# Kernel tuning notes

Hardware: AMD Instinct MI355X
Metric: run time of the kernel (lower is better)

Reference implementation:

```python
import jax, jax.numpy as jnp
import numpy as np

B, H, D = 2048, 4, 4096   # batch, num_heads_h, dim
M = 8                      # groups_m

def setup_inputs() -> dict:
    key = jax.random.key(0)
    ks = jax.random.split(key, 5)
    return {
        "x": jax.random.normal(ks[0], (B, H, D), dtype=jnp.float32),
        "local_W": jax.random.normal(ks[1], (M, H), dtype=jnp.float32) * 0.5,
        "local_b": jax.random.normal(ks[2], (M,), dtype=jnp.float32) * 0.02,
        "proj_W": jax.random.normal(ks[3], (D, D), dtype=jnp.float32) * 0.02,
        "proj_b": jax.random.normal(ks[4], (D,), dtype=jnp.float32) * 0.02,
    }

def reference(x, local_W, local_b, proj_W, proj_b):
    b, h, d = x.shape
    m = local_W.shape[0]
    dm = d // m
    # s: (m, B, dm, h)  -- matches reshape(B,h,m,-1).permute(2,0,3,1)
    s = jnp.transpose(x.reshape(b, h, m, dm), (2, 0, 3, 1))
    # grouped tiny linear (Linear(h,1) per group), all fused in one einsum
    s_out = jnp.einsum('mbch,mh->mbc', s, local_W) + local_b[:, None, None]
    # faithful to torch: cat along dim 0 then reshape(B, D) (group-major flatten)
    s_out = s_out.reshape(b, d)
    out = jax.nn.sigmoid(s_out @ proj_W.T + proj_b)
    return out
```

## Files before the change

### kernel.cpp

```cpp
#include <hip/hip_runtime.h>


#define MD 2048
#define ND 4096
#define KD 4096

typedef __attribute__((ext_vector_type(8))) __bf16 bf16x8;
typedef __attribute__((ext_vector_type(4))) float f32x4;

static __device__ __forceinline__ unsigned short f2bf(float f) {
  union { float f; unsigned int u; } v; v.f = f;
  unsigned int u = v.u;
  u += 0x7FFFu + ((u >> 16) & 1u);
  return (unsigned short)(u >> 16);
}

__global__ __launch_bounds__(256) void prep_kernel(
    const float* __restrict__ x, const float* __restrict__ lW,
    const float* __restrict__ lb, const float* __restrict__ pW,
    unsigned short* __restrict__ sB, unsigned short* __restrict__ wB) {
  int bid = blockIdx.x;
  int tid = threadIdx.x;
  if (bid < 4096) {
    int g = bid * 256 + tid;
    int j8 = g << 3;
    int r = j8 >> 12;
    int j = j8 & 4095;
    int m = r >> 8;
    int b = ((r & 255) << 3) + (j >> 9);
    int c = j & 511;
    const float* xp = x + ((long)b << 14) + m * 512 + c;
    float w0 = lW[m * 4 + 0], w1 = lW[m * 4 + 1], w2 = lW[m * 4 + 2], w3 = lW[m * 4 + 3];
    float bb = lb[m];
    float4 xa0 = *(const float4*)(xp);
    float4 xb0 = *(const float4*)(xp + 4);
    float4 xa1 = *(const float4*)(xp + 4096);
    float4 xb1 = *(const float4*)(xp + 4100);
    float4 xa2 = *(const float4*)(xp + 8192);
    float4 xb2 = *(const float4*)(xp + 8196);
    float4 xa3 = *(const float4*)(xp + 12288);
    float4 xb3 = *(const float4*)(xp + 12292);
    float v0 = bb + xa0.x * w0 + xa1.x * w1 + xa2.x * w2 + xa3.x * w3;
    float v1 = bb + xa0.y * w0 + xa1.y * w1 + xa2.y * w2 + xa3.y * w3;
    float v2 = bb + xa0.z * w0 + xa1.z * w1 + xa2.z * w2 + xa3.z * w3;
    float v3 = bb + xa0.w * w0 + xa1.w * w1 + xa2.w * w2 + xa3.w * w3;
    float v4 = bb + xb0.x * w0 + xb1.x * w1 + xb2.x * w2 + xb3.x * w3;
    float v5 = bb + xb0.y * w0 + xb1.y * w1 + xb2.y * w2 + xb3.y * w3;
    float v6 = bb + xb0.z * w0 + xb1.z * w1 + xb2.z * w2 + xb3.z * w3;
    float v7 = bb + xb0.w * w0 + xb1.w * w1 + xb2.w * w2 + xb3.w * w3;
    uint4 pk;
    pk.x = (unsigned)f2bf(v0) | ((unsigned)f2bf(v1) << 16);
    pk.y = (unsigned)f2bf(v2) | ((unsigned)f2bf(v3) << 16);
    pk.z = (unsigned)f2bf(v4) | ((unsigned)f2bf(v5) << 16);
    pk.w = (unsigned)f2bf(v6) | ((unsigned)f2bf(v7) << 16);
    *(uint4*)(sB + j8) = pk;
  } else {
    int g = (bid - 4096) * 256 + tid;
    long off = (long)g << 4;
    float4 a = *(const float4*)(pW + off);
    float4 b4 = *(const float4*)(pW + off + 4);
    float4 c4 = *(const float4*)(pW + off + 8);
    float4 d4 = *(const float4*)(pW + off + 12);
    uint4 p0, p1;
    p0.x = (unsigned)f2bf(a.x) | ((unsigned)f2bf(a.y) << 16);
    p0.y = (unsigned)f2bf(a.z) | ((unsigned)f2bf(a.w) << 16);
    p0.z = (unsigned)f2bf(b4.x) | ((unsigned)f2bf(b4.y) << 16);
    p0.w = (unsigned)f2bf(b4.z) | ((unsigned)f2bf(b4.w) << 16);
    p1.x = (unsigned)f2bf(c4.x) | ((unsigned)f2bf(c4.y) << 16);
    p1.y = (unsigned)f2bf(c4.z) | ((unsigned)f2bf(c4.w) << 16);
    p1.z = (unsigned)f2bf(d4.x) | ((unsigned)f2bf(d4.y) << 16);
    p1.w = (unsigned)f2bf(d4.z) | ((unsigned)f2bf(d4.w) << 16);
    *(uint4*)(wB + off) = p0;
    *(uint4*)(wB + off + 8) = p1;
  }
}

#define BM 128
#define BN 128
#define BK 64

__global__ __launch_bounds__(256) void gemm_kernel(
    const unsigned short* __restrict__ S, const unsigned short* __restrict__ W,
    const float* __restrict__ pb, float* __restrict__ out) {
  __shared__ unsigned short As[BM * BK];
  __shared__ unsigned short Bs[BN * BK];
  int tid = threadIdx.x;
  int lane = tid & 63;
  int wave = tid >> 6;
  int n0 = blockIdx.x * BN;
  int r0 = blockIdx.y * BM;
  int wr = wave >> 1, wc = wave & 1;

  int srow = (wave << 5) + (lane >> 3);
  int scol = (((lane & 7) ^ (lane >> 3)) << 3);
  const unsigned short* gA = S + (long)(r0 + srow) * KD + scol;
  const unsigned short* gB = W + (long)(n0 + srow) * KD + scol;
  unsigned short* lA = &As[(wave << 5) * BK];
  unsigned short* lB = &Bs[(wave << 5) * BK];

  f32x4 acc[4][4] = {};

  for (int kt = 0; kt < KD; kt += BK) {
    __syncthreads();
#pragma unroll
    for (int i = 0; i < 4; ++i) {
      __builtin_amdgcn_global_load_lds(
          (const __attribute__((address_space(1))) unsigned int*)(gA + (long)i * 8 * KD + kt),
          (__attribute__((address_space(3))) unsigned int*)(lA + i * 8 * BK), 16, 0, 0);
      __builtin_amdgcn_global_load_lds(
          (const __attribute__((address_space(1))) unsigned int*)(gB + (long)i * 8 * KD + kt),
          (__attribute__((address_space(3))) unsigned int*)(lB + i * 8 * BK), 16, 0, 0);
    }
    __syncthreads();
#pragma unroll
    for (int ks = 0; ks < 2; ++ks) {
      int swz = (((ks << 2) + (lane >> 4)) ^ (lane & 7)) << 3;
      bf16x8 af[4], bfr[4];
#pragma unroll
      for (int t = 0; t < 4; ++t) {
        af[t]  = *(const bf16x8*)&As[((wr << 6) + t * 16 + (lane & 15)) * BK + swz];
        bfr[t] = *(const bf16x8*)&Bs[((wc << 6) + t * 16 + (lane & 15)) * BK + swz];
      }
#pragma unroll
      for (int mt = 0; mt < 4; ++mt)
#pragma unroll
        for (int nt = 0; nt < 4; ++nt)
          acc[mt][nt] = __builtin_amdgcn_mfma_f32_16x16x32_bf16(af[mt], bfr[nt], acc[mt][nt], 0, 0, 0);
    }
  }

#pragma unroll
  for (int nt = 0; nt < 4; ++nt) {
    int col = n0 + (wc << 6) + nt * 16 + (lane & 15);
    float pbv = pb[col];
#pragma unroll
    for (int mt = 0; mt < 4; ++mt) {
      int row = r0 + (wr << 6) + mt * 16 + ((lane >> 4) << 2);
#pragma unroll
      for (int i = 0; i < 4; ++i) {
        float v = acc[mt][nt][i] + pbv;
        out[(long)(row + i) * ND + col] = 1.0f / (1.0f + __expf(-v));
      }
    }
  }
}

extern "C" void kernel_launch(void* const* d_in, const int* in_sizes, int n_in,
                              void* d_out, int out_size, void* d_ws, size_t ws_size,
                              hipStream_t stream) {
  const float* x  = (const float*)d_in[0];
  const float* lW = (const float*)d_in[1];
  const float* lb = (const float*)d_in[2];
  const float* pW = (const float*)d_in[3];
  const float* pb = (const float*)d_in[4];
  float* out = (float*)d_out;

  unsigned short* sB = (unsigned short*)d_ws;
  unsigned short* wB = sB + (long)MD * KD;

  prep_kernel<<<8192, 256, 0, stream>>>(x, lW, lb, pW, sB, wB);
  gemm_kernel<<<dim3(32, 16), 256, 0, stream>>>(sB, wB, pb, out);
}
```

Baseline: 320.4 us.

## Fuse proj_W fp32-to-bf16 conversion into GEMM tile loading

Removes the separate pass that converted proj_W to a bf16 workspace. The GEMM now streams fp32 W tiles into LDS (prefetched one K-step ahead), converts them to bf16 in LDS, then runs the MFMAs. This saves the extra read and write of the 64MB weight, but each W tile is now re-read in fp32 by all 16 row-blocks. That doubles W's L2/HBM traffic inside the GEMM and adds LDS usage and conversion work to the main loop.

```diff
diff --git a/kernel.cpp b/kernel.cpp
--- a/kernel.cpp
+++ b/kernel.cpp
@@ -8,71 +8,48 @@
 typedef __attribute__((ext_vector_type(8))) __bf16 bf16x8;
 typedef __attribute__((ext_vector_type(4))) float f32x4;
 
-static __device__ __forceinline__ unsigned short f2bf(float f) {
+static __device__ __forceinline__ unsigned int f2bf(float f) {
   union { float f; unsigned int u; } v; v.f = f;
   unsigned int u = v.u;
   u += 0x7FFFu + ((u >> 16) & 1u);
-  return (unsigned short)(u >> 16);
+  return u >> 16;
 }
 
 __global__ __launch_bounds__(256) void prep_kernel(
     const float* __restrict__ x, const float* __restrict__ lW,
-    const float* __restrict__ lb, const float* __restrict__ pW,
-    unsigned short* __restrict__ sB, unsigned short* __restrict__ wB) {
-  int bid = blockIdx.x;
-  int tid = threadIdx.x;
-  if (bid < 4096) {
-    int g = bid * 256 + tid;
-    int j8 = g << 3;
-    int r = j8 >> 12;
-    int j = j8 & 4095;
-    int m = r >> 8;
-    int b = ((r & 255) << 3) + (j >> 9);
-    int c = j & 511;
-    const float* xp = x + ((long)b << 14) + m * 512 + c;
-    float w0 = lW[m * 4 + 0], w1 = lW[m * 4 + 1], w2 = lW[m * 4 + 2], w3 = lW[m * 4 + 3];
-    float bb = lb[m];
-    float4 xa0 = *(const float4*)(xp);
-    float4 xb0 = *(const float4*)(xp + 4);
-    float4 xa1 = *(const float4*)(xp + 4096);
-    float4 xb1 = *(const float4*)(xp + 4100);
-    float4 xa2 = *(const float4*)(xp + 8192);
-    float4 xb2 = *(const float4*)(xp + 8196);
-    float4 xa3 = *(const float4*)(xp + 12288);
-    float4 xb3 = *(const float4*)(xp + 12292);
-    float v0 = bb + xa0.x * w0 + xa1.x * w1 + xa2.x * w2 + xa3.x * w3;
-    float v1 = bb + xa0.y * w0 + xa1.y * w1 + xa2.y * w2 + xa3.y * w3;
-    float v2 = bb + xa0.z * w0 + xa1.z * w1 + xa2.z * w2 + xa3.z * w3;
-    float v3 = bb + xa0.w * w0 + xa1.w * w1 + xa2.w * w2 + xa3.w * w3;
-    float v4 = bb + xb0.x * w0 + xb1.x * w1 + xb2.x * w2 + xb3.x * w3;
-    float v5 = bb + xb0.y * w0 + xb1.y * w1 + xb2.y * w2 + xb3.y * w3;
-    float v6 = bb + xb0.z * w0 + xb1.z * w1 + xb2.z * w2 + xb3.z * w3;
-    float v7 = bb + xb0.w * w0 + xb1.w * w1 + xb2.w * w2 + xb3.w * w3;
-    uint4 pk;
-    pk.x = (unsigned)f2bf(v0) | ((unsigned)f2bf(v1) << 16);
-    pk.y = (unsigned)f2bf(v2) | ((unsigned)f2bf(v3) << 16);
-    pk.z = (unsigned)f2bf(v4) | ((unsigned)f2bf(v5) << 16);
-    pk.w = (unsigned)f2bf(v6) | ((unsigned)f2bf(v7) << 16);
-    *(uint4*)(sB + j8) = pk;
-  } else {
-    int g = (bid - 4096) * 256 + tid;
-    long off = (long)g << 4;
-    float4 a = *(const float4*)(pW + off);
-    float4 b4 = *(const float4*)(pW + off + 4);
-    float4 c4 = *(const float4*)(pW + off + 8);
-    float4 d4 = *(const float4*)(pW + off + 12);
-    uint4 p0, p1;
-    p0.x = (unsigned)f2bf(a.x) | ((unsigned)f2bf(a.y) << 16);
-    p0.y = (unsigned)f2bf(a.z) | ((unsigned)f2bf(a.w) << 16);
-    p0.z = (unsigned)f2bf(b4.x) | ((unsigned)f2bf(b4.y) << 16);
-    p0.w = (unsigned)f2bf(b4.z) | ((unsigned)f2bf(b4.w) << 16);
-    p1.x = (unsigned)f2bf(c4.x) | ((unsigned)f2bf(c4.y) << 16);
-    p1.y = (unsigned)f2bf(c4.z) | ((unsigned)f2bf(c4.w) << 16);
-    p1.z = (unsigned)f2bf(d4.x) | ((unsigned)f2bf(d4.y) << 16);
-    p1.w = (unsigned)f2bf(d4.z) | ((unsigned)f2bf(d4.w) << 16);
-    *(uint4*)(wB + off) = p0;
-    *(uint4*)(wB + off + 8) = p1;
-  }
+    const float* __restrict__ lb, unsigned short* __restrict__ sB) {
+  int g = blockIdx.x * 256 + threadIdx.x;
+  int j8 = g << 3;
+  int r = j8 >> 12;
+  int j = j8 & 4095;
+  int m = r >> 8;
+  int b = ((r & 255) << 3) + (j >> 9);
+  int c = j & 511;
+  const float* xp = x + ((long)b << 14) + m * 512 + c;
+  float w0 = lW[m * 4 + 0], w1 = lW[m * 4 + 1], w2 = lW[m * 4 + 2], w3 = lW[m * 4 + 3];
+  float bb = lb[m];
+  float4 xa0 = *(const float4*)(xp);
+  float4 xb0 = *(const float4*)(xp + 4);
+  float4 xa1 = *(const float4*)(xp + 4096);
+  float4 xb1 = *(const float4*)(xp + 4100);
+  float4 xa2 = *(const float4*)(xp + 8192);
+  float4 xb2 = *(const float4*)(xp + 8196);
+  float4 xa3 = *(const float4*)(xp + 12288);
+  float4 xb3 = *(const float4*)(xp + 12292);
+  float v0 = bb + xa0.x * w0 + xa1.x * w1 + xa2.x * w2 + xa3.x * w3;
+  float v1 = bb + xa0.y * w0 + xa1.y * w1 + xa2.y * w2 + xa3.y * w3;
+  float v2 = bb + xa0.z * w0 + xa1.z * w1 + xa2.z * w2 + xa3.z * w3;
+  float v3 = bb + xa0.w * w0 + xa1.w * w1 + xa2.w * w2 + xa3.w * w3;
+  float v4 = bb + xb0.x * w0 + xb1.x * w1 + xb2.x * w2 + xb3.x * w3;
+  float v5 = bb + xb0.y * w0 + xb1.y * w1 + xb2.y * w2 + xb3.y * w3;
+  float v6 = bb + xb0.z * w0 + xb1.z * w1 + xb2.z * w2 + xb3.z * w3;
+  float v7 = bb + xb0.w * w0 + xb1.w * w1 + xb2.w * w2 + xb3.w * w3;
+  uint4 pk;
+  pk.x = f2bf(v0) | (f2bf(v1) << 16);
+  pk.y = f2bf(v2) | (f2bf(v3) << 16);
+  pk.z = f2bf(v4) | (f2bf(v5) << 16);
+  pk.w = f2bf(v6) | (f2bf(v7) << 16);
+  *(uint4*)(sB + j8) = pk;
 }
 
 #define BM 128
@@ -80,10 +57,11 @@
 #define BK 64
 
 __global__ __launch_bounds__(256) void gemm_kernel(
-    const unsigned short* __restrict__ S, const unsigned short* __restrict__ W,
+    const unsigned short* __restrict__ S, const float* __restrict__ W,
     const float* __restrict__ pb, float* __restrict__ out) {
   __shared__ unsigned short As[BM * BK];
   __shared__ unsigned short Bs[BN * BK];
+  __shared__ float B32[BN * BK];
   int tid = threadIdx.x;
   int lane = tid & 63;
   int wave = tid >> 6;
@@ -94,24 +72,62 @@
   int srow = (wave << 5) + (lane >> 3);
   int scol = (((lane & 7) ^ (lane >> 3)) << 3);
   const unsigned short* gA = S + (long)(r0 + srow) * KD + scol;
-  const unsigned short* gB = W + (long)(n0 + srow) * KD + scol;
   unsigned short* lA = &As[(wave << 5) * BK];
-  unsigned short* lB = &Bs[(wave << 5) * BK];
+
+  const float* Wn0 = W + (long)n0 * KD;
+  int boff[8];
+#pragma unroll
+  for (int i = 0; i < 8; ++i) {
+    int c = (i << 8) + tid;
+    int row = c >> 4;
+    boff[i] = row * KD + (((c & 15) ^ (row & 15)) << 2);
+  }
+
+  int brow = tid >> 1;
+  int bh8 = (tid & 1) << 3;
+  int bswz15 = brow & 15;
+  int bswz7 = brow & 7;
+  const float* rB32 = B32 + brow * BK;
+  unsigned short* wBs = &Bs[brow * BK];
 
   f32x4 acc[4][4] = {};
+
+#pragma unroll
+  for (int i = 0; i < 8; ++i)
+    __builtin_amdgcn_global_load_lds(
+        (const __attribute__((address_space(1))) unsigned int*)(Wn0 + boff[i]),
+        (__attribute__((address_space(3))) unsigned int*)(B32 + (((i << 8) + (wave << 6)) << 2)),
+        16, 0, 0);
 
   for (int kt = 0; kt < KD; kt += BK) {
     __syncthreads();
 #pragma unroll
-    for (int i = 0; i < 4; ++i) {
+    for (int i = 0; i < 4; ++i)
       __builtin_amdgcn_global_load_lds(
           (const __attribute__((address_space(1))) unsigned int*)(gA + (long)i * 8 * KD + kt),
           (__attribute__((address_space(3))) unsigned int*)(lA + i * 8 * BK), 16, 0, 0);
-      __builtin_amdgcn_global_load_lds(
-          (const __attribute__((address_space(1))) unsigned int*)(gB + (long)i * 8 * KD + kt),
-          (__attribute__((address_space(3))) unsigned int*)(lB + i * 8 * BK), 16, 0, 0);
+#pragma unroll
+    for (int qq = 0; qq < 4; ++qq) {
+      int q0 = 2 * qq, q1 = 2 * qq + 1;
+      f32x4 u = *(const f32x4*)(rB32 + (((bh8 + q0) ^ bswz15) << 2));
+      f32x4 v = *(const f32x4*)(rB32 + (((bh8 + q1) ^ bswz15) << 2));
+      uint4 pk;
+      pk.x = f2bf(u[0]) | (f2bf(u[1]) << 16);
+      pk.y = f2bf(u[2]) | (f2bf(u[3]) << 16);
+      pk.z = f2bf(v[0]) | (f2bf(v[1]) << 16);
+      pk.w = f2bf(v[2]) | (f2bf(v[3]) << 16);
+      *(uint4*)&wBs[((((bh8 >> 1) + qq) ^ bswz7) << 3)] = pk;
     }
     __syncthreads();
+    if (kt + BK < KD) {
+      int ktn = kt + BK;
+#pragma unroll
+      for (int i = 0; i < 8; ++i)
+        __builtin_amdgcn_global_load_lds(
+            (const __attribute__((address_space(1))) unsigned int*)(Wn0 + boff[i] + ktn),
+            (__attribute__((address_space(3))) unsigned int*)(B32 + (((i << 8) + (wave << 6)) << 2)),
+            16, 0, 0);
+    }
 #pragma unroll
     for (int ks = 0; ks < 2; ++ks) {
       int swz = (((ks << 2) + (lane >> 4)) ^ (lane & 7)) << 3;
@@ -156,8 +172,7 @@
   float* out = (float*)d_out;
 
   unsigned short* sB = (unsigned short*)d_ws;
-  unsigned short* wB = sB + (long)MD * KD;
 
-  prep_kernel<<<8192, 256, 0, stream>>>(x, lW, lb, pW, sB, wB);
-  gemm_kernel<<<dim3(32, 16), 256, 0, stream>>>(sB, wB, pb, out);
+  prep_kernel<<<4096, 256, 0, stream>>>(x, lW, lb, sB);
+  gemm_kernel<<<dim3(32, 16), 256, 0, stream>>>(sB, pW, pb, out);
 }
```

Measured after the change: 348.3 us. 1.09x slower.

## Triple-buffer LDS pipeline with 128x256 tiles and 8 waves in bf16 GEMM

Applied to the files above, without the earlier changes.

Widens the GEMM tile to 128x256 with 512 threads (8 waves, 2x4 layout) and adds a three-stage LDS ring buffer. Each tile's global-to-LDS loads are issued two iterations ahead, so memory traffic overlaps MFMA work. Explicit vmcnt/lgkmcnt waits, barriers and s_setprio interleave fragment loads and MFMA bursts across waves. LDS use grows to about 144KB per block, and the grid halves to 256 blocks, which could lower occupancy and leave some CUs idle.

```diff
diff --git a/kernel.cpp b/kernel.cpp
--- a/kernel.cpp
+++ b/kernel.cpp
@@ -76,56 +76,92 @@
 }
 
 #define BM 128
-#define BN 128
+#define BN 256
 #define BK 64
-
-__global__ __launch_bounds__(256) void gemm_kernel(
+#define NT (KD / BK)
+
+__global__ __launch_bounds__(512) void gemm_kernel(
     const unsigned short* __restrict__ S, const unsigned short* __restrict__ W,
     const float* __restrict__ pb, float* __restrict__ out) {
-  __shared__ unsigned short As[BM * BK];
-  __shared__ unsigned short Bs[BN * BK];
+  __shared__ unsigned short As[3][BM * BK];
+  __shared__ unsigned short Bs[3][BN * BK];
   int tid = threadIdx.x;
   int lane = tid & 63;
   int wave = tid >> 6;
   int n0 = blockIdx.x * BN;
   int r0 = blockIdx.y * BM;
-  int wr = wave >> 1, wc = wave & 1;
-
-  int srow = (wave << 5) + (lane >> 3);
-  int scol = (((lane & 7) ^ (lane >> 3)) << 3);
-  const unsigned short* gA = S + (long)(r0 + srow) * KD + scol;
-  const unsigned short* gB = W + (long)(n0 + srow) * KD + scol;
-  unsigned short* lA = &As[(wave << 5) * BK];
-  unsigned short* lB = &Bs[(wave << 5) * BK];
+  int wr = wave >> 2;
+  int wc = wave & 3;
+
+  int strow = tid >> 3;
+  int sgoff = (((tid & 7) ^ ((tid >> 3) & 7)) << 3);
+  const unsigned short* gA = S + (long)(r0 + strow) * KD + sgoff;
+  const unsigned short* gB = W + (long)(n0 + strow) * KD + sgoff;
+
+#define STAGE(pbuf, tt) do {                                                   \
+    const long ko_ = (long)(tt) * BK;                                          \
+    _Pragma("unroll")                                                          \
+    for (int i_ = 0; i_ < 2; ++i_)                                             \
+      __builtin_amdgcn_global_load_lds(                                        \
+          (const __attribute__((address_space(1))) unsigned int*)(gA + (long)i_ * 64 * KD + ko_), \
+          (__attribute__((address_space(3))) unsigned int*)(&As[pbuf][(i_ * 64 + (wave << 3)) * BK]), 16, 0, 0); \
+    _Pragma("unroll")                                                          \
+    for (int i_ = 0; i_ < 4; ++i_)                                             \
+      __builtin_amdgcn_global_load_lds(                                        \
+          (const __attribute__((address_space(1))) unsigned int*)(gB + (long)i_ * 64 * KD + ko_), \
+          (__attribute__((address_space(3))) unsigned int*)(&Bs[pbuf][(i_ * 64 + (wave << 3)) * BK]), 16, 0, 0); \
+  } while (0)
+
+#define LOADFRAG(pp, av, bv, ksv) do {                                         \
+    int swz_ = ((((ksv) << 2) + (lane >> 4)) ^ (lane & 7)) << 3;               \
+    _Pragma("unroll")                                                          \
+    for (int t_ = 0; t_ < 4; ++t_) {                                           \
+      av[t_] = *(const bf16x8*)&As[pp][((wr << 6) + t_ * 16 + (lane & 15)) * BK + swz_]; \
+      bv[t_] = *(const bf16x8*)&Bs[pp][((wc << 6) + t_ * 16 + (lane & 15)) * BK + swz_]; \
+    }                                                                          \
+  } while (0)
+
+#define MFMA16(av, bv) do {                                                    \
+    _Pragma("unroll")                                                          \
+    for (int mt_ = 0; mt_ < 4; ++mt_)                                          \
+      _Pragma("unroll")                                                        \
+      for (int nt_ = 0; nt_ < 4; ++nt_)                                        \
+        acc[mt_][nt_] = __builtin_amdgcn_mfma_f32_16x16x32_bf16(               \
+            av[mt_], bv[nt_], acc[mt_][nt_], 0, 0, 0);                         \
+  } while (0)
 
   f32x4 acc[4][4] = {};
 
-  for (int kt = 0; kt < KD; kt += BK) {
-    __syncthreads();
-#pragma unroll
-    for (int i = 0; i < 4; ++i) {
-      __builtin_amdgcn_global_load_lds(
-          (const __attribute__((address_space(1))) unsigned int*)(gA + (long)i * 8 * KD + kt),
-          (__attribute__((address_space(3))) unsigned int*)(lA + i * 8 * BK), 16, 0, 0);
-      __builtin_amdgcn_global_load_lds(
-          (const __attribute__((address_space(1))) unsigned int*)(gB + (long)i * 8 * KD + kt),
-          (__attribute__((address_space(3))) unsigned int*)(lB + i * 8 * BK), 16, 0, 0);
-    }
-    __syncthreads();
-#pragma unroll
-    for (int ks = 0; ks < 2; ++ks) {
-      int swz = (((ks << 2) + (lane >> 4)) ^ (lane & 7)) << 3;
-      bf16x8 af[4], bfr[4];
-#pragma unroll
-      for (int t = 0; t < 4; ++t) {
-        af[t]  = *(const bf16x8*)&As[((wr << 6) + t * 16 + (lane & 15)) * BK + swz];
-        bfr[t] = *(const bf16x8*)&Bs[((wc << 6) + t * 16 + (lane & 15)) * BK + swz];
+  STAGE(0, 0);
+  STAGE(1, 1);
+  asm volatile("s_waitcnt vmcnt(6)" ::: "memory");
+  __builtin_amdgcn_s_barrier();
+
+  for (int t = 0; t < NT; ++t) {
+    const int p = t % 3;
+    bf16x8 a0[4], b0[4];
+    LOADFRAG(p, a0, b0, 0);
+    if (t + 2 < NT) STAGE((t + 2) % 3, t + 2);
+    __builtin_amdgcn_s_barrier();
+    asm volatile("s_waitcnt lgkmcnt(0)" ::: "memory");
+    __builtin_amdgcn_s_setprio(1);
+    MFMA16(a0, b0);
+    __builtin_amdgcn_s_setprio(0);
+    __builtin_amdgcn_s_barrier();
+    bf16x8 a1[4], b1[4];
+    LOADFRAG(p, a1, b1, 1);
+    __builtin_amdgcn_s_barrier();
+    asm volatile("s_waitcnt lgkmcnt(0)" ::: "memory");
+    __builtin_amdgcn_s_setprio(1);
+    MFMA16(a1, b1);
+    __builtin_amdgcn_s_setprio(0);
+    if (t + 1 < NT) {
+      if (t + 2 < NT) {
+        asm volatile("s_waitcnt vmcnt(6)" ::: "memory");
+      } else {
+        asm volatile("s_waitcnt vmcnt(0)" ::: "memory");
       }
-#pragma unroll
-      for (int mt = 0; mt < 4; ++mt)
-#pragma unroll
-        for (int nt = 0; nt < 4; ++nt)
-          acc[mt][nt] = __builtin_amdgcn_mfma_f32_16x16x32_bf16(af[mt], bfr[nt], acc[mt][nt], 0, 0, 0);
+      __builtin_amdgcn_s_barrier();
     }
   }
 
@@ -143,6 +179,9 @@
       }
     }
   }
+#undef STAGE
+#undef LOADFRAG
+#undef MFMA16
 }
 
 extern "C" void kernel_launch(void* const* d_in, const int* in_sizes, int n_in,
@@ -159,5 +198,5 @@
   unsigned short* wB = sB + (long)MD * KD;
 
   prep_kernel<<<8192, 256, 0, stream>>>(x, lW, lb, pW, sB, wB);
-  gemm_kernel<<<dim3(32, 16), 256, 0, stream>>>(sB, wB, pb, out);
-}
+  gemm_kernel<<<dim3(16, 16), 512, 0, stream>>>(sB, wB, pb, out);
+}
```

Measured after the change: 331.3 us. 1.03x slower.

## Double-buffer LDS tiles, enlarge M tile to 256, and remap block ids

Applied to the files above, without the earlier changes.

The GEMM now keeps two LDS buffers for A and B. The global-to-LDS load of the next K tile is issued before computing on the current one, leaving one barrier per iteration instead of two. The M tile doubles to 256 rows, so each wave computes an 8x4 grid of MFMA tiles, which raises reuse of the B fragments. Block ids are remapped on a 1D grid of 256 blocks to group tiles for better cache locality. The cost is one block per CU with only 4 waves, more LDS and accumulator registers, and the stage still depends on the barrier to wait for the async loads.

```diff
diff --git a/kernel.cpp b/kernel.cpp
--- a/kernel.cpp
+++ b/kernel.cpp
@@ -75,57 +75,67 @@
   }
 }
 
-#define BM 128
+#define BM 256
 #define BN 128
 #define BK 64
 
 __global__ __launch_bounds__(256) void gemm_kernel(
     const unsigned short* __restrict__ S, const unsigned short* __restrict__ W,
     const float* __restrict__ pb, float* __restrict__ out) {
-  __shared__ unsigned short As[BM * BK];
-  __shared__ unsigned short Bs[BN * BK];
+  __shared__ unsigned short As[2][BM * BK];
+  __shared__ unsigned short Bs[2][BN * BK];
   int tid = threadIdx.x;
   int lane = tid & 63;
   int wave = tid >> 6;
-  int n0 = blockIdx.x * BN;
-  int r0 = blockIdx.y * BM;
+
+  int bid = blockIdx.x;
+  int wg = ((bid & 7) << 5) + (bid >> 3);
+  int r0 = (wg >> 5) << 8;
+  int n0 = (wg & 31) << 7;
   int wr = wave >> 1, wc = wave & 1;
 
-  int srow = (wave << 5) + (lane >> 3);
+  int srow = (wave << 3) + (lane >> 3);
   int scol = (((lane & 7) ^ (lane >> 3)) << 3);
   const unsigned short* gA = S + (long)(r0 + srow) * KD + scol;
   const unsigned short* gB = W + (long)(n0 + srow) * KD + scol;
-  unsigned short* lA = &As[(wave << 5) * BK];
-  unsigned short* lB = &Bs[(wave << 5) * BK];
 
-  f32x4 acc[4][4] = {};
+#define STAGE(buf, tt) do {                                                    \
+    const long ko_ = (long)(tt) * BK;                                          \
+    _Pragma("unroll")                                                          \
+    for (int i_ = 0; i_ < 8; ++i_)                                             \
+      __builtin_amdgcn_global_load_lds(                                        \
+          (const __attribute__((address_space(1))) unsigned int*)(gA + (long)i_ * 32 * KD + ko_), \
+          (__attribute__((address_space(3))) unsigned int*)(&As[buf][(i_ * 32 + (wave << 3)) * BK]), 16, 0, 0); \
+    _Pragma("unroll")                                                          \
+    for (int i_ = 0; i_ < 4; ++i_)                                             \
+      __builtin_amdgcn_global_load_lds(                                        \
+          (const __attribute__((address_space(1))) unsigned int*)(gB + (long)i_ * 32 * KD + ko_), \
+          (__attribute__((address_space(3))) unsigned int*)(&Bs[buf][(i_ * 32 + (wave << 3)) * BK]), 16, 0, 0); \
+  } while (0)
 
-  for (int kt = 0; kt < KD; kt += BK) {
+  f32x4 acc[8][4] = {};
+
+  STAGE(0, 0);
+
+  for (int t = 0; t < KD / BK; ++t) {
     __syncthreads();
-#pragma unroll
-    for (int i = 0; i < 4; ++i) {
-      __builtin_amdgcn_global_load_lds(
-          (const __attribute__((address_space(1))) unsigned int*)(gA + (long)i * 8 * KD + kt),
-          (__attribute__((address_space(3))) unsigned int*)(lA + i * 8 * BK), 16, 0, 0);
-      __builtin_amdgcn_global_load_lds(
-          (const __attribute__((address_space(1))) unsigned int*)(gB + (long)i * 8 * KD + kt),
-          (__attribute__((address_space(3))) unsigned int*)(lB + i * 8 * BK), 16, 0, 0);
-    }
-    __syncthreads();
+    if (t + 1 < KD / BK) STAGE((t + 1) & 1, t + 1);
+    int cur = t & 1;
 #pragma unroll
     for (int ks = 0; ks < 2; ++ks) {
       int swz = (((ks << 2) + (lane >> 4)) ^ (lane & 7)) << 3;
-      bf16x8 af[4], bfr[4];
+      bf16x8 af[8], bfv[4];
 #pragma unroll
-      for (int t = 0; t < 4; ++t) {
-        af[t]  = *(const bf16x8*)&As[((wr << 6) + t * 16 + (lane & 15)) * BK + swz];
-        bfr[t] = *(const bf16x8*)&Bs[((wc << 6) + t * 16 + (lane & 15)) * BK + swz];
-      }
+      for (int mt = 0; mt < 8; ++mt)
+        af[mt] = *(const bf16x8*)&As[cur][((wr << 7) + mt * 16 + (lane & 15)) * BK + swz];
 #pragma unroll
-      for (int mt = 0; mt < 4; ++mt)
+      for (int nt = 0; nt < 4; ++nt)
+        bfv[nt] = *(const bf16x8*)&Bs[cur][((wc << 6) + nt * 16 + (lane & 15)) * BK + swz];
+#pragma unroll
+      for (int mt = 0; mt < 8; ++mt)
 #pragma unroll
         for (int nt = 0; nt < 4; ++nt)
-          acc[mt][nt] = __builtin_amdgcn_mfma_f32_16x16x32_bf16(af[mt], bfr[nt], acc[mt][nt], 0, 0, 0);
+          acc[mt][nt] = __builtin_amdgcn_mfma_f32_16x16x32_bf16(af[mt], bfv[nt], acc[mt][nt], 0, 0, 0);
     }
   }
 
@@ -134,8 +144,8 @@
     int col = n0 + (wc << 6) + nt * 16 + (lane & 15);
     float pbv = pb[col];
 #pragma unroll
-    for (int mt = 0; mt < 4; ++mt) {
-      int row = r0 + (wr << 6) + mt * 16 + ((lane >> 4) << 2);
+    for (int mt = 0; mt < 8; ++mt) {
+      int row = r0 + (wr << 7) + mt * 16 + ((lane >> 4) << 2);
 #pragma unroll
       for (int i = 0; i < 4; ++i) {
         float v = acc[mt][nt][i] + pbv;
@@ -143,6 +153,7 @@
       }
     }
   }
+#undef STAGE
 }
 
 extern "C" void kernel_launch(void* const* d_in, const int* in_sizes, int n_in,
@@ -159,5 +170,5 @@
   unsigned short* wB = sB + (long)MD * KD;
 
   prep_kernel<<<8192, 256, 0, stream>>>(x, lW, lb, pW, sB, wB);
-  gemm_kernel<<<dim3(32, 16), 256, 0, stream>>>(sB, wB, pb, out);
+  gemm_kernel<<<256, 256, 0, stream>>>(sB, wB, pb, out);
 }
```

Result: slower. 377.9 us (+17.9%).
